# Kernel tuning notes

Hardware: AMD Instinct MI355X
Metric: run time of the kernel (lower is better)

The kernel has to match this reference:

```python
import jax, jax.numpy as jnp
import numpy as np
import math

D_MODEL = 1024
NUM_HEADS = 16
THETA = 10000.0


def _rope(x, pos, theta):
    # x: (B, S, H, d_k), pos: (B, S) int32/64
    d_k = x.shape[-1]
    half = d_k // 2
    inv_freq = theta ** (-jnp.arange(half, dtype=jnp.float32) * 2.0 / d_k)  # (half,)
    ang = pos.astype(jnp.float32)[..., None] * inv_freq  # (B, S, half)
    cos = jnp.cos(ang)[..., None, :]  # (B, S, 1, half) broadcast over heads
    sin = jnp.sin(ang)[..., None, :]
    x1 = x[..., 0::2]  # even dims
    x2 = x[..., 1::2]  # odd dims
    out_even = x1 * cos - x2 * sin
    out_odd = x1 * sin + x2 * cos
    # re-interleave pairs
    return jnp.stack([out_even, out_odd], axis=-1).reshape(x.shape)


def setup_inputs() -> dict:
    key = jax.random.key(0)
    k0, k1, k2, k3, k4 = jax.random.split(key, 5)
    B, S, D = 4, 2048, D_MODEL
    std = math.sqrt(2.0 / (D + D))
    x = jax.random.normal(k0, (B, S, D), dtype=jnp.float32)
    wq = jax.random.normal(k1, (D, D), dtype=jnp.float32) * std
    wk = jax.random.normal(k2, (D, D), dtype=jnp.float32) * std
    wv = jax.random.normal(k3, (D, D), dtype=jnp.float32) * std
    wo = jax.random.normal(k4, (D, D), dtype=jnp.float32) * std
    return {"x": x, "wq": wq, "wk": wk, "wv": wv, "wo": wo}


def reference(x, wq, wk, wv, wo):
    B, S, D = x.shape
    H = NUM_HEADS
    d_k = D // H
    # torch Linear: y = x @ W.T
    q = (x @ wq.T).reshape(B, S, H, d_k)
    k = (x @ wk.T).reshape(B, S, H, d_k)
    v = (x @ wv.T).reshape(B, S, H, d_k)
    pos = jnp.broadcast_to(jnp.arange(S), (B, S))
    q = _rope(q, pos, THETA)
    k = _rope(k, pos, THETA)
    # (B, H, S, d_k)
    q = q.transpose(0, 2, 1, 3)
    k = k.transpose(0, 2, 1, 3)
    v = v.transpose(0, 2, 1, 3)
    scores = jnp.einsum("bhqd,bhkd->bhqk", q, k) / jnp.sqrt(jnp.float32(d_k))
    causal = jnp.tril(jnp.ones((S, S), dtype=bool))  # True = keep
    scores = jnp.where(causal, scores, -jnp.inf)
    attn = jax.nn.softmax(scores, axis=-1)
    out = jnp.einsum("bhqk,bhkd->bhqd", attn, v)
    out = out.transpose(0, 2, 1, 3).reshape(B, S, D)
    return out @ wo.T
```

## Files before the change

### kernel.cpp

```cpp
#include <hip/hip_runtime.h>

#define DEV __device__ __forceinline__

typedef float f32x4 __attribute__((ext_vector_type(4)));
typedef float f32x16 __attribute__((ext_vector_type(16)));
typedef __bf16 bf16x8 __attribute__((ext_vector_type(8)));
typedef unsigned u32x4 __attribute__((ext_vector_type(4)));
typedef unsigned short u16x8 __attribute__((ext_vector_type(8)));

static constexpr int BB = 4, SS = 2048, DD = 1024, HH = 16;
static constexpr int MM = BB * SS;
static constexpr float LOG2_THETA_OVER_HALF = 0.4152410118609203f;
static constexpr float SCL2 = 0.18033688011112042f;

DEV unsigned short f2b(float f) {
    unsigned u = __float_as_uint(f);
    unsigned r = (u + 0x7fffu + ((u >> 16) & 1u)) >> 16;
    return (unsigned short)r;
}
DEV float b2f(unsigned short h) { return __uint_as_float(((unsigned)h) << 16); }

DEV void gload16(const void* g, void* l) {
    __builtin_amdgcn_global_load_lds((const __attribute__((address_space(1))) void*)g,
                                     (__attribute__((address_space(3))) void*)l, 16, 0, 0);
}

DEV unsigned cvtpk(float lo, float hi) {
    unsigned r;
    asm("v_cvt_pk_bf16_f32 %0, %1, %2" : "=v"(r) : "v"(lo), "v"(hi));
    return r;
}

#define PH_BAR do { __builtin_amdgcn_sched_barrier(0); __builtin_amdgcn_s_barrier(); __builtin_amdgcn_sched_barrier(0); } while (0)

__global__ void k_f2b(const float* __restrict__ src, unsigned short* __restrict__ dst, int n) {
    int i = (blockIdx.x * blockDim.x + threadIdx.x) * 4;
    if (i >= n) return;
    float4 v = *reinterpret_cast<const float4*>(src + i);
    ushort4 o;
    o.x = f2b(v.x); o.y = f2b(v.y); o.z = f2b(v.z); o.w = f2b(v.w);
    *reinterpret_cast<ushort4*>(dst + i) = o;
}

__global__ void k_f2b4(const float* __restrict__ s0, const float* __restrict__ s1,
                       const float* __restrict__ s2, const float* __restrict__ s3,
                       unsigned short* __restrict__ dst) {
    int bid = blockIdx.x;
    int t = bid >> 10;
    const float* src = (t == 0) ? s0 : (t == 1) ? s1 : (t == 2) ? s2 : s3;
    int i = ((bid & 1023) * 256 + threadIdx.x) * 4;
    float4 v = *reinterpret_cast<const float4*>(src + i);
    ushort4 o;
    o.x = f2b(v.x); o.y = f2b(v.y); o.z = f2b(v.z); o.w = f2b(v.w);
    *reinterpret_cast<ushort4*>(dst + (size_t)t * DD * DD + i) = o;
}

__global__ __launch_bounds__(512, 2) void k_gemm8(const unsigned short* __restrict__ A,
                                                  const unsigned short* __restrict__ Bw,
                                                  unsigned short* __restrict__ C, int ldc) {
    __shared__ __align__(16) unsigned short LdsA[4][128 * 64];
    __shared__ __align__(16) unsigned short LdsB[4][128 * 64];
    const int tid = threadIdx.x, lane = tid & 63, wid = tid >> 6;
    const int wm = wid >> 2, wn = wid & 3;
    const int fr = lane & 15, l4 = lane >> 4, sw = fr & 7;
    const int m0 = blockIdx.y * 256, n0 = blockIdx.x * 256;

    const int r0 = tid >> 3;
    const int cg = (tid & 7) ^ (r0 & 7);
    const unsigned short* aS = A  + (size_t)(m0 + r0) * 1024 + (cg << 3);
    const unsigned short* bS = Bw + (size_t)(n0 + r0) * 1024 + (cg << 3);
    unsigned short* dA = &LdsA[0][0];
    unsigned short* dB = &LdsB[0][0];
    const int dOf = wid * 512;

    f32x4 acc[8][4] = {};

#define STG(src, base, slot) do {                         \
        unsigned short* d_ = (base) + (slot) * 8192 + dOf;\
        gload16((src), d_);                               \
        gload16((src) + 64 * 1024, d_ + 4096);            \
    } while (0)

#pragma unroll
    for (int T = 0; T < 2; ++T) {
        STG(bS + T * 64,          dB, (2 * T) & 3);
        STG(bS + T * 64 + 131072, dB, (2 * T + 1) & 3);
        STG(aS + T * 64,          dA, (2 * T) & 3);
        STG(aS + T * 64 + 131072, dA, (2 * T + 1) & 3);
    }

    bf16x8 aF[4][2], bL[2][2], bH[2][2];

    for (int T = 0; T < 16; ++T) {
        if (T < 15) { asm volatile("s_waitcnt vmcnt(8)" ::: "memory"); }
        else        { asm volatile("s_waitcnt vmcnt(0)" ::: "memory"); }
        PH_BAR;

        const unsigned short* As_ = &LdsA[(2 * T + wm) & 3][0];
        const unsigned short* Bs_ = &LdsB[(2 * T + (wn >> 1)) & 3][0];
        const int bro = (wn & 1) * 64;

#pragma unroll
        for (int m = 0; m < 4; ++m)
#pragma unroll
            for (int kk = 0; kk < 2; ++kk)
                aF[m][kk] = *(const bf16x8*)&As_[(m * 16 + fr) * 64 + ((((kk << 2) | l4) ^ sw) << 3)];
#pragma unroll
        for (int n = 0; n < 2; ++n)
#pragma unroll
            for (int kk = 0; kk < 2; ++kk)
                bL[n][kk] = *(const bf16x8*)&Bs_[(bro + n * 16 + fr) * 64 + ((((kk << 2) | l4) ^ sw) << 3)];
        PH_BAR;
        __builtin_amdgcn_s_setprio(1);
#pragma unroll
        for (int m = 0; m < 4; ++m)
#pragma unroll
            for (int n = 0; n < 2; ++n)
#pragma unroll
                for (int kk = 0; kk < 2; ++kk)
                    acc[m][n] = __builtin_amdgcn_mfma_f32_16x16x32_bf16(aF[m][kk], bL[n][kk], acc[m][n], 0, 0, 0);
        __builtin_amdgcn_s_setprio(0);
        PH_BAR;

#pragma unroll
        for (int n = 0; n < 2; ++n)
#pragma unroll
            for (int kk = 0; kk < 2; ++kk)
                bH[n][kk] = *(const bf16x8*)&Bs_[(bro + (n + 2) * 16 + fr) * 64 + ((((kk << 2) | l4) ^ sw) << 3)];
        PH_BAR;
        __builtin_amdgcn_s_setprio(1);
#pragma unroll
        for (int m = 0; m < 4; ++m)
#pragma unroll
            for (int n = 0; n < 2; ++n)
#pragma unroll
                for (int kk = 0; kk < 2; ++kk)
                    acc[m][n + 2] = __builtin_amdgcn_mfma_f32_16x16x32_bf16(aF[m][kk], bH[n][kk], acc[m][n + 2], 0, 0, 0);
        __builtin_amdgcn_s_setprio(0);
        PH_BAR;

#pragma unroll
        for (int m = 0; m < 4; ++m)
#pragma unroll
            for (int kk = 0; kk < 2; ++kk)
                aF[m][kk] = *(const bf16x8*)&As_[((m + 4) * 16 + fr) * 64 + ((((kk << 2) | l4) ^ sw) << 3)];
        if (T + 2 < 16) {
            STG(bS + (T + 2) * 64,          dB, (2 * T) & 3);
            STG(bS + (T + 2) * 64 + 131072, dB, (2 * T + 1) & 3);
        }
        PH_BAR;
        __builtin_amdgcn_s_setprio(1);
#pragma unroll
        for (int m = 0; m < 4; ++m)
#pragma unroll
            for (int n = 0; n < 2; ++n)
#pragma unroll
                for (int kk = 0; kk < 2; ++kk)
                    acc[m + 4][n + 2] = __builtin_amdgcn_mfma_f32_16x16x32_bf16(aF[m][kk], bH[n][kk], acc[m + 4][n + 2], 0, 0, 0);
        __builtin_amdgcn_s_setprio(0);
        PH_BAR;

        if (T + 2 < 16) {
            STG(aS + (T + 2) * 64,          dA, (2 * T) & 3);
            STG(aS + (T + 2) * 64 + 131072, dA, (2 * T + 1) & 3);
        }
        PH_BAR;
        __builtin_amdgcn_s_setprio(1);
#pragma unroll
        for (int m = 0; m < 4; ++m)
#pragma unroll
            for (int n = 0; n < 2; ++n)
#pragma unroll
                for (int kk = 0; kk < 2; ++kk)
                    acc[m + 4][n] = __builtin_amdgcn_mfma_f32_16x16x32_bf16(aF[m][kk], bL[n][kk], acc[m + 4][n], 0, 0, 0);
        __builtin_amdgcn_s_setprio(0);
    }
#undef STG

    const int rb = l4 * 4;
#pragma unroll
    for (int m = 0; m < 8; ++m)
#pragma unroll
        for (int n = 0; n < 4; ++n)
#pragma unroll
            for (int r = 0; r < 4; ++r) {
                int row = m0 + wm * 128 + m * 16 + rb + r;
                int col = n0 + wn * 64 + n * 16 + fr;
                C[(size_t)row * ldc + col] = f2b(acc[m][n][r]);
            }
}

template <int OUTF32>
__global__ __launch_bounds__(256) void k_gemm(const unsigned short* __restrict__ A,
                                              const unsigned short* __restrict__ Bw,
                                              void* __restrict__ Cp, int ldc) {
    __shared__ __align__(16) unsigned short As[128 * 32];
    __shared__ __align__(16) unsigned short Bs[128 * 32];
    const int tid = threadIdx.x;
    const int lane = tid & 63, wid = tid >> 6;
    const int wm = wid >> 1, wn = wid & 1;
    const int fr = lane & 15, fk8 = (lane >> 4) * 8;
    const int m0 = blockIdx.y * 128, n0 = blockIdx.x * 128;
    const int r0 = tid >> 2, c0 = (tid & 3) * 8;

    f32x4 acc[4][4] = {};

    for (int kt = 0; kt < 1024; kt += 32) {
        gload16(&A[(size_t)(m0 + r0) * 1024 + kt + c0],       (unsigned short*)As + wid * 512);
        gload16(&A[(size_t)(m0 + 64 + r0) * 1024 + kt + c0],  (unsigned short*)As + 2048 + wid * 512);
        gload16(&Bw[(size_t)(n0 + r0) * 1024 + kt + c0],      (unsigned short*)Bs + wid * 512);
        gload16(&Bw[(size_t)(n0 + 64 + r0) * 1024 + kt + c0], (unsigned short*)Bs + 2048 + wid * 512);
        __syncthreads();

        bf16x8 af[4], bfv[4];
#pragma unroll
        for (int i = 0; i < 4; i++)
            af[i] = *(const bf16x8*)&As[(wm * 64 + i * 16 + fr) * 32 + fk8];
#pragma unroll
        for (int j = 0; j < 4; j++)
            bfv[j] = *(const bf16x8*)&Bs[(wn * 64 + j * 16 + fr) * 32 + fk8];
#pragma unroll
        for (int i = 0; i < 4; i++)
#pragma unroll
            for (int j = 0; j < 4; j++)
                acc[i][j] = __builtin_amdgcn_mfma_f32_16x16x32_bf16(af[i], bfv[j], acc[i][j], 0, 0, 0);
        __syncthreads();
    }

    const int rb = (lane >> 4) * 4;
#pragma unroll
    for (int i = 0; i < 4; i++)
#pragma unroll
        for (int j = 0; j < 4; j++)
#pragma unroll
            for (int r = 0; r < 4; r++) {
                int row = m0 + wm * 64 + i * 16 + rb + r;
                int col = n0 + wn * 64 + j * 16 + fr;
                if (OUTF32) ((float*)Cp)[(size_t)row * ldc + col] = acc[i][j][r];
                else        ((unsigned short*)Cp)[(size_t)row * ldc + col] = f2b(acc[i][j][r]);
            }
}

__global__ void k_ropeQK(unsigned short* __restrict__ T) {
    int g = blockIdx.x * blockDim.x + threadIdx.x;
    int m = g >> 9, p = g & 511;
    int i = p & 31;
    int s = m & (SS - 1);
    int col = ((p >> 5) << 6) + (i << 1);
    float inv = exp2f(-(float)i * LOG2_THETA_OVER_HALF);
    float ang = (float)s * inv;
    float sn, cs;
    sincosf(ang, &sn, &cs);
    unsigned short* q2 = T + (size_t)m * 3072 + col;
    unsigned short* k2 = q2 + 1024;
    float q1 = b2f(q2[0]), q2v = b2f(q2[1]);
    float k1 = b2f(k2[0]), k2v = b2f(k2[1]);
    q2[0] = f2b((q1 * cs - q2v * sn) * SCL2);
    q2[1] = f2b((q1 * sn + q2v * cs) * SCL2);
    k2[0] = f2b(k1 * cs - k2v * sn);
    k2[1] = f2b(k1 * sn + k2v * cs);
}

__global__ __launch_bounds__(256) void k_vt(const unsigned short* __restrict__ V,
                                            unsigned short* __restrict__ Vt) {
    __shared__ unsigned short T[64 * 65];
    const int tid = threadIdx.x;
    const int s0 = blockIdx.x * 64, bh = blockIdx.y;
    const int b = bh >> 4, h = bh & 15;
    const int r = tid >> 3, c8 = (tid & 7) * 8;
#pragma unroll
    for (int p = 0; p < 2; p++) {
        int row = p * 32 + r;
        u16x8 v = *(const u16x8*)&V[(size_t)(b * SS + s0 + row) * 3072 + h * 64 + c8];
#pragma unroll
        for (int j = 0; j < 8; j++) T[(c8 + j) * 65 + row] = v[j];
    }
    __syncthreads();
#pragma unroll
    for (int p = 0; p < 2; p++) {
        int d = p * 32 + r;
        u16x8 o;
#pragma unroll
        for (int j = 0; j < 8; j++) o[j] = T[d * 65 + c8 + j];
        *(u16x8*)&Vt[((size_t)bh * 64 + d) * 2048 + s0 + c8] = o;
    }
}

DEV void packp(const f32x16& s, bf16x8* pf) {
#pragma unroll
    for (int g = 0; g < 2; g++) {
        unsigned w0 = cvtpk(s[8 * g + 0], s[8 * g + 1]);
        unsigned w1 = cvtpk(s[8 * g + 2], s[8 * g + 3]);
        unsigned w2 = cvtpk(s[8 * g + 4], s[8 * g + 5]);
        unsigned w3 = cvtpk(s[8 * g + 6], s[8 * g + 7]);
        asm("v_permlane32_swap_b32 %0, %1" : "+v"(w0), "+v"(w2));
        asm("v_permlane32_swap_b32 %0, %1" : "+v"(w1), "+v"(w3));
        u32x4 pd;
        pd[0] = w0; pd[1] = w1; pd[2] = w2; pd[3] = w3;
        pf[g] = __builtin_bit_cast(bf16x8, pd);
    }
}

DEV float sum16(const f32x16& s) {
    return (((s[0] + s[1]) + (s[2] + s[3])) + ((s[4] + s[5]) + (s[6] + s[7]))) +
           (((s[8] + s[9]) + (s[10] + s[11])) + (((s[12] + s[13]) + (s[14] + s[15]))));
}

__global__ __launch_bounds__(512, 4) void k_attn(const unsigned short* __restrict__ QKV,
                                                 const unsigned short* __restrict__ Vt,
                                                 unsigned short* __restrict__ O) {
    __shared__ __align__(16) unsigned short Kbuf[2][64 * 64];
    __shared__ __align__(16) unsigned short Vbuf[2][64 * 64];
    const int tid = threadIdx.x, lane = tid & 63, wid = tid >> 6;
    const int l31 = lane & 31, hi = lane >> 5;
    const int bh = blockIdx.x, b = bh >> 4, h = bh & 15;
    const int qt = gridDim.y - 1 - blockIdx.y;
    const int q0 = qt * 256;
    const int wq0 = q0 + wid * 32;
    const int tdw = wq0 >> 6;
    const int nk = (q0 + 256) >> 6;

    const int srow = tid >> 3, sc = tid & 7;
    const unsigned short* ksrc = QKV + 1024 + ((size_t)(b * SS) + srow) * 3072 + h * 64 + ((sc ^ (srow & 7)) << 3);
    const unsigned short* vsrc = Vt + ((size_t)(bh * 64) + srow) * 2048 + ((sc ^ (srow & 7)) << 3);

    const unsigned short* qp = QKV + (size_t)(b * SS + wq0 + l31) * 3072 + h * 64;
    bf16x8 qf[4];
#pragma unroll
    for (int dt = 0; dt < 4; dt++) qf[dt] = *(const bf16x8*)(qp + dt * 16 + hi * 8);

    f32x16 oacc0 = {}, oacc1 = {};
    float lrow = 0.f;
    const int swz = l31 & 7;

    gload16(ksrc, (unsigned short*)Kbuf[0] + wid * 512);
    gload16(vsrc, (unsigned short*)Vbuf[0] + wid * 512);

    for (int t = 0; t < nk; t++) {
        __syncthreads();
        if (t + 1 < nk) {
            gload16(ksrc + (size_t)(t + 1) * 64 * 3072, (unsigned short*)Kbuf[(t + 1) & 1] + wid * 512);
            gload16(vsrc + (t + 1) * 64,                (unsigned short*)Vbuf[(t + 1) & 1] + wid * 512);
        }
        if (t > tdw) continue;
        const unsigned short* Ks = Kbuf[t & 1];
        const unsigned short* Vs = Vbuf[t & 1];

        if (t < tdw) {
            f32x16 s0 = {}, s1 = {};
            __builtin_amdgcn_s_setprio(1);
#pragma unroll
            for (int dt = 0; dt < 4; dt++) {
                bf16x8 kf = *(const bf16x8*)&Ks[l31 * 64 + (((dt * 2 + hi) ^ swz) << 3)];
                s0 = __builtin_amdgcn_mfma_f32_32x32x16_bf16(kf, qf[dt], s0, 0, 0, 0);
            }
#pragma unroll
            for (int dt = 0; dt < 4; dt++) {
                bf16x8 kf = *(const bf16x8*)&Ks[(32 + l31) * 64 + (((dt * 2 + hi) ^ swz) << 3)];
                s1 = __builtin_amdgcn_mfma_f32_32x32x16_bf16(kf, qf[dt], s1, 0, 0, 0);
            }
            __builtin_amdgcn_s_setprio(0);
#pragma unroll
            for (int r = 0; r < 16; r++) {
                s0[r] = __builtin_amdgcn_exp2f(s0[r]);
                s1[r] = __builtin_amdgcn_exp2f(s1[r]);
            }
            lrow += sum16(s0) + sum16(s1);
            bf16x8 pA[2], pB[2];
            packp(s0, pA);
            packp(s1, pB);
            __builtin_amdgcn_s_setprio(1);
#pragma unroll
            for (int g = 0; g < 2; g++) {
                bf16x8 vf0 = *(const bf16x8*)&Vs[l31 * 64 + (((g * 2 + hi) ^ swz) << 3)];
                oacc0 = __builtin_amdgcn_mfma_f32_32x32x16_bf16(vf0, pA[g], oacc0, 0, 0, 0);
                bf16x8 vf1 = *(const bf16x8*)&Vs[(32 + l31) * 64 + (((g * 2 + hi) ^ swz) << 3)];
                oacc1 = __builtin_amdgcn_mfma_f32_32x32x16_bf16(vf1, pA[g], oacc1, 0, 0, 0);
            }
#pragma unroll
            for (int g = 0; g < 2; g++) {
                bf16x8 vf0 = *(const bf16x8*)&Vs[l31 * 64 + (((4 + g * 2 + hi) ^ swz) << 3)];
                oacc0 = __builtin_amdgcn_mfma_f32_32x32x16_bf16(vf0, pB[g], oacc0, 0, 0, 0);
                bf16x8 vf1 = *(const bf16x8*)&Vs[(32 + l31) * 64 + (((4 + g * 2 + hi) ^ swz) << 3)];
                oacc1 = __builtin_amdgcn_mfma_f32_32x32x16_bf16(vf1, pB[g], oacc1, 0, 0, 0);
            }
            __builtin_amdgcn_s_setprio(0);
        } else {
#pragma unroll
            for (int kt2 = 0; kt2 < 2; kt2++) {
                const int kb = t * 64 + kt2 * 32;
                if (kb > wq0) break;

                f32x16 sacc = {};
                __builtin_amdgcn_s_setprio(1);
#pragma unroll
                for (int dt = 0; dt < 4; dt++) {
                    bf16x8 kf = *(const bf16x8*)&Ks[(kt2 * 32 + l31) * 64 + (((dt * 2 + hi) ^ swz) << 3)];
                    sacc = __builtin_amdgcn_mfma_f32_32x32x16_bf16(kf, qf[dt], sacc, 0, 0, 0);
                }
                __builtin_amdgcn_s_setprio(0);

                if (kb == wq0) {
#pragma unroll
                    for (int r = 0; r < 16; r++) {
                        int kr = (r & 3) + 8 * (r >> 2) + 4 * hi;
                        sacc[r] = (kr > l31) ? -1e30f : sacc[r];
                    }
                }

#pragma unroll
                for (int r = 0; r < 16; r++) sacc[r] = __builtin_amdgcn_exp2f(sacc[r]);
                lrow += sum16(sacc);

                bf16x8 pf[2];
                packp(sacc, pf);

                __builtin_amdgcn_s_setprio(1);
#pragma unroll
                for (int g = 0; g < 2; g++) {
                    bf16x8 vf0 = *(const bf16x8*)&Vs[l31 * 64 + (((kt2 * 4 + g * 2 + hi) ^ swz) << 3)];
                    oacc0 = __builtin_amdgcn_mfma_f32_32x32x16_bf16(vf0, pf[g], oacc0, 0, 0, 0);
                    bf16x8 vf1 = *(const bf16x8*)&Vs[(32 + l31) * 64 + (((kt2 * 4 + g * 2 + hi) ^ swz) << 3)];
                    oacc1 = __builtin_amdgcn_mfma_f32_32x32x16_bf16(vf1, pf[g], oacc1, 0, 0, 0);
                }
                __builtin_amdgcn_s_setprio(0);
            }
        }
    }

    float lsum = lrow + __shfl_xor(lrow, 32);
    float linv = 1.0f / lsum;
    unsigned short* op = O + (size_t)(b * SS + wq0 + l31) * 1024 + h * 64 + hi * 4;
#pragma unroll
    for (int g = 0; g < 4; g++) {
        uint2 u;
        u.x = cvtpk(oacc0[4 * g + 0] * linv, oacc0[4 * g + 1] * linv);
        u.y = cvtpk(oacc0[4 * g + 2] * linv, oacc0[4 * g + 3] * linv);
        *(uint2*)&op[g * 8] = u;
        uint2 v;
        v.x = cvtpk(oacc1[4 * g + 0] * linv, oacc1[4 * g + 1] * linv);
        v.y = cvtpk(oacc1[4 * g + 2] * linv, oacc1[4 * g + 3] * linv);
        *(uint2*)&op[32 + g * 8] = v;
    }
}

extern "C" void kernel_launch(void* const* d_in, const int* in_sizes, int n_in,
                              void* d_out, int out_size, void* d_ws, size_t ws_size,
                              hipStream_t stream) {
    const float* x  = (const float*)d_in[0];
    const float* wq = (const float*)d_in[1];
    const float* wk = (const float*)d_in[2];
    const float* wv = (const float*)d_in[3];
    const float* wo = (const float*)d_in[4];
    float* out = (float*)d_out;

    unsigned short* xb    = (unsigned short*)d_ws;
    unsigned short* wqkvb = xb + (size_t)MM * DD;
    unsigned short* wob   = wqkvb + (size_t)3 * DD * DD;
    unsigned short* QKV   = wob + (size_t)DD * DD;
    unsigned short* Ob    = QKV + (size_t)MM * 3 * DD;
    unsigned short* Vtb   = xb;

    k_f2b<<<MM * DD / 4 / 256, 256, 0, stream>>>(x, xb, MM * DD);
    k_f2b4<<<4096, 256, 0, stream>>>(wq, wk, wv, wo, wqkvb);

    dim3 gq(3 * DD / 256, MM / 256);
    k_gemm8<<<gq, 512, 0, stream>>>(xb, wqkvb, QKV, 3 * DD);

    int npair = MM * 512;
    k_ropeQK<<<npair / 256, 256, 0, stream>>>(QKV);

    dim3 gv(SS / 64, BB * HH);
    k_vt<<<gv, 256, 0, stream>>>(QKV + 2 * DD, Vtb);

    dim3 ga(BB * HH, SS / 256);
    k_attn<<<ga, 512, 0, stream>>>(QKV, Vtb, Ob);

    dim3 gg(DD / 128, MM / 128);
    k_gemm<1><<<gg, 256, 0, stream>>>(Ob, wob, (void*)out, DD);
}
```

Baseline: 182.1 us.

## Stagger GEMM tile loads into half-stages with A prefetched one step ahead

Restructures the global-to-LDS prefetch schedule of the 256x256 bf16 GEMM. Each tile load is split into half-tile chunks spread over the four MFMA phases. A is now fetched one k-step ahead while B stays two steps ahead, the vmcnt wait is tightened to match, and an explicit lgkmcnt(0) wait is added before each MFMA block. The aim is to spread memory issue more evenly across the loop and reduce bursts that contend with LDS reads. The cost is a shorter prefetch distance for A, which may expose more global-load latency.

```diff
diff --git a/kernel.cpp b/kernel.cpp
--- a/kernel.cpp
+++ b/kernel.cpp
@@ -32,6 +32,7 @@
 }
 
 #define PH_BAR do { __builtin_amdgcn_sched_barrier(0); __builtin_amdgcn_s_barrier(); __builtin_amdgcn_sched_barrier(0); } while (0)
+#define LGKM0  do { asm volatile("s_waitcnt lgkmcnt(0)" ::: "memory"); __builtin_amdgcn_sched_barrier(0); } while (0)
 
 __global__ void k_f2b(const float* __restrict__ src, unsigned short* __restrict__ dst, int n) {
     int i = (blockIdx.x * blockDim.x + threadIdx.x) * 4;
@@ -75,24 +76,21 @@
 
     f32x4 acc[8][4] = {};
 
-#define STG(src, base, slot) do {                         \
-        unsigned short* d_ = (base) + (slot) * 8192 + dOf;\
-        gload16((src), d_);                               \
-        gload16((src) + 64 * 1024, d_ + 4096);            \
+#define STGH(src, base, t, h) do {                                          \
+        unsigned short* d_ = (base) + (((2 * (t) + (h)) & 3) * 8192) + dOf; \
+        const unsigned short* s_ = (src) + (size_t)(t) * 64 + (size_t)(h) * 131072; \
+        gload16(s_, d_);                                                    \
+        gload16(s_ + 65536, d_ + 4096);                                     \
     } while (0)
 
-#pragma unroll
-    for (int T = 0; T < 2; ++T) {
-        STG(bS + T * 64,          dB, (2 * T) & 3);
-        STG(bS + T * 64 + 131072, dB, (2 * T + 1) & 3);
-        STG(aS + T * 64,          dA, (2 * T) & 3);
-        STG(aS + T * 64 + 131072, dA, (2 * T + 1) & 3);
-    }
+    STGH(bS, dB, 0, 0); STGH(bS, dB, 0, 1);
+    STGH(aS, dA, 0, 0); STGH(aS, dA, 0, 1);
+    STGH(bS, dB, 1, 0); STGH(bS, dB, 1, 1);
 
     bf16x8 aF[4][2], bL[2][2], bH[2][2];
 
     for (int T = 0; T < 16; ++T) {
-        if (T < 15) { asm volatile("s_waitcnt vmcnt(8)" ::: "memory"); }
+        if (T < 15) { asm volatile("s_waitcnt vmcnt(4)" ::: "memory"); }
         else        { asm volatile("s_waitcnt vmcnt(0)" ::: "memory"); }
         PH_BAR;
 
@@ -110,7 +108,9 @@
 #pragma unroll
             for (int kk = 0; kk < 2; ++kk)
                 bL[n][kk] = *(const bf16x8*)&Bs_[(bro + n * 16 + fr) * 64 + ((((kk << 2) | l4) ^ sw) << 3)];
-        PH_BAR;
+        if (T + 1 < 16) STGH(aS, dA, T + 1, 0);
+        PH_BAR;
+        LGKM0;
         __builtin_amdgcn_s_setprio(1);
 #pragma unroll
         for (int m = 0; m < 4; ++m)
@@ -127,7 +127,9 @@
 #pragma unroll
             for (int kk = 0; kk < 2; ++kk)
                 bH[n][kk] = *(const bf16x8*)&Bs_[(bro + (n + 2) * 16 + fr) * 64 + ((((kk << 2) | l4) ^ sw) << 3)];
-        PH_BAR;
+        if (T + 1 < 16) STGH(aS, dA, T + 1, 1);
+        PH_BAR;
+        LGKM0;
         __builtin_amdgcn_s_setprio(1);
 #pragma unroll
         for (int m = 0; m < 4; ++m)
@@ -144,11 +146,9 @@
 #pragma unroll
             for (int kk = 0; kk < 2; ++kk)
                 aF[m][kk] = *(const bf16x8*)&As_[((m + 4) * 16 + fr) * 64 + ((((kk << 2) | l4) ^ sw) << 3)];
-        if (T + 2 < 16) {
-            STG(bS + (T + 2) * 64,          dB, (2 * T) & 3);
-            STG(bS + (T + 2) * 64 + 131072, dB, (2 * T + 1) & 3);
-        }
-        PH_BAR;
+        if (T + 2 < 16) STGH(bS, dB, T + 2, 0);
+        PH_BAR;
+        LGKM0;
         __builtin_amdgcn_s_setprio(1);
 #pragma unroll
         for (int m = 0; m < 4; ++m)
@@ -160,10 +160,7 @@
         __builtin_amdgcn_s_setprio(0);
         PH_BAR;
 
-        if (T + 2 < 16) {
-            STG(aS + (T + 2) * 64,          dA, (2 * T) & 3);
-            STG(aS + (T + 2) * 64 + 131072, dA, (2 * T + 1) & 3);
-        }
+        if (T + 2 < 16) STGH(bS, dB, T + 2, 1);
         PH_BAR;
         __builtin_amdgcn_s_setprio(1);
 #pragma unroll
@@ -175,7 +172,7 @@
                     acc[m + 4][n] = __builtin_amdgcn_mfma_f32_16x16x32_bf16(aF[m][kk], bL[n][kk], acc[m + 4][n], 0, 0, 0);
         __builtin_amdgcn_s_setprio(0);
     }
-#undef STG
+#undef STGH
 
     const int rb = l4 * 4;
 #pragma unroll
```

Result: slower. 186.3 us (+2.3%).
